# Optimization experiments

Hardware: AMD Instinct MI355X
Metric: run time of the kernel (lower is better)

## Reference

```python
import jax, jax.numpy as jnp
import numpy as np

S, B, C, H, M = 384, 8, 1024, 16, 1536
CC = C // H


def setup_inputs() -> dict:
    key = jax.random.key(0)
    ks = jax.random.split(key, 8)
    x = jax.random.normal(ks[0], (S, B, C), dtype=jnp.float32)
    pe = jax.random.normal(ks[1], (S, B, C), dtype=jnp.float32)
    memory_k = jax.random.normal(ks[2], (M, B, H, CC), dtype=jnp.float32)
    memory_v = jax.random.normal(ks[3], (M, B, H, CC), dtype=jnp.float32)
    w_qkv = jax.random.normal(ks[4], (C, 3 * C), dtype=jnp.float32) * 0.02
    b_qkv = jnp.zeros((3 * C,), dtype=jnp.float32)
    w_out = jax.random.normal(ks[5], (C, C), dtype=jnp.float32) * 0.02
    b_out = jnp.zeros((C,), dtype=jnp.float32)
    terminal = jnp.zeros((B,), dtype=bool)
    # causal mask over the new tokens: True = masked (future positions)
    content_mask = jnp.broadcast_to(
        (jnp.arange(S)[None, :] > jnp.arange(S)[:, None])[:, :, None], (S, S, B))
    padding_mask = jnp.zeros((S, B), dtype=bool)  # True = padded
    memory_length = jax.random.randint(ks[6], (B,), 0, M, dtype=jnp.int32)
    return dict(x=x, positional_encoding=pe, memory_k=memory_k, memory_v=memory_v,
                w_qkv=w_qkv, b_qkv=b_qkv, w_out=w_out, b_out=b_out,
                terminal=terminal, content_mask=content_mask,
                padding_mask=padding_mask, memory_length=memory_length)


def reference(x, positional_encoding, memory_k, memory_v, w_qkv, b_qkv,
              w_out, b_out, terminal, content_mask, padding_mask, memory_length):
    s, b, c = x.shape
    # qkv projection
    qkv = (x + positional_encoding) @ w_qkv + b_qkv          # [s,b,3c]
    q, k, v = jnp.split(qkv, 3, axis=-1)
    q = q.reshape(s, b, H, CC)
    k = k.reshape(s, b, H, CC)
    v = v.reshape(s, b, H, CC)
    # clear_memory(terminal): zero lengths for terminal episodes
    mem_len = jnp.where(terminal, 0, memory_length)          # [b]
    # ragged memory concat expressed with fixed capacity M + padding mask
    k_full = jnp.concatenate([memory_k, k], axis=0)          # [M+s,b,H,CC]
    v_full = jnp.concatenate([memory_v, v], axis=0)
    mem_pad = jnp.arange(M)[:, None] >= mem_len[None, :]     # [M,b] True=masked
    kv_pad = jnp.concatenate([mem_pad, padding_mask], axis=0)  # [M+s,b]
    mem_content = jnp.zeros((s, M, b), dtype=bool)           # memory visible to all queries
    full_content = jnp.concatenate([mem_content, content_mask], axis=1)  # [s,M+s,b]
    mask = full_content | kv_pad[None, :, :]                 # [s,M+s,b]
    # attention
    scores = jnp.einsum('sbhc,tbhc->stbh', q, k_full) * (1.0 / np.sqrt(CC))
    scores = jnp.where(mask[:, :, :, None], jnp.float32(-1e9), scores)
    p = jax.nn.softmax(scores, axis=1)                       # [s,M+s,b,h]
    out = jnp.einsum('stbh,tbhc->sbhc', p, v_full).reshape(s, b, c)
    return out @ w_out + b_out
```

## Files before the change

kernel.cpp:

```cpp
#include <hip/hip_runtime.h>
#include <math.h>

#define S_DIM 384
#define B_DIM 8
#define C_DIM 1024
#define H_DIM 16
#define M_DIM 1536
#define CC_DIM 64
#define ROWS  (S_DIM * B_DIM)
#define N3C   (3 * C_DIM)
#define CHUNK 6
#define MAXS  5

typedef unsigned short u16;
typedef short bf8v  __attribute__((ext_vector_type(8)));
typedef short bf4v  __attribute__((ext_vector_type(4)));
typedef u16   us8   __attribute__((ext_vector_type(8)));
typedef u16   us4   __attribute__((ext_vector_type(4)));
typedef float f4v   __attribute__((ext_vector_type(4)));

__device__ __forceinline__ u16 f2bf(float f) {
    unsigned u = __float_as_uint(f);
    u += 0x7fffu + ((u >> 16) & 1u);
    return (u16)(u >> 16);
}
__device__ __forceinline__ float bf2f(u16 v) {
    return __uint_as_float(((unsigned)v) << 16);
}
#if __has_builtin(__builtin_amdgcn_exp2f)
#define EX2(x) __builtin_amdgcn_exp2f(x)
#else
#define EX2(x) __expf((x) * 0.69314718056f)
#endif
#define QSCALE (0.125f * 1.44269504f)

__device__ __forceinline__ f4v mfma16x16x16bf16(bf4v a, bf4v b, f4v c) {
#if __has_builtin(__builtin_amdgcn_mfma_f32_16x16x16bf16_1k)
    return __builtin_amdgcn_mfma_f32_16x16x16bf16_1k(a, b, c, 0, 0, 0);
#else
    return c;
#endif
}

__device__ __forceinline__ void gload16(const u16* g, u16* l) {
    __builtin_amdgcn_global_load_lds(
        (const __attribute__((address_space(1))) void*)g,
        (__attribute__((address_space(3))) void*)l, 16, 0, 0);
}

__device__ __forceinline__ void tr_direct8(const float* __restrict__ in,
                                           u16* __restrict__ out,
                                           int R, int Cc, int r0, int c0, int tid) {
    const int c4 = c0 + (tid & 15) * 4;
    const int rq = r0 + (tid >> 4) * 8;
    float4 L[8];
    #pragma unroll
    for (int k = 0; k < 8; k++)
        L[k] = *(const float4*)(in + (size_t)(rq + k) * Cc + c4);
    #pragma unroll
    for (int j = 0; j < 4; j++) {
        us8 o;
        #pragma unroll
        for (int k = 0; k < 8; k++)
            o[k] = f2bf(((const float*)&L[k])[j]);
        *(us8*)(out + (size_t)(c4 + j) * R + rq) = o;
    }
}

__global__ __launch_bounds__(256) void prep_all(
    const float* __restrict__ x, const float* __restrict__ pe, u16* __restrict__ Abf,
    const float* __restrict__ wqkv, u16* __restrict__ Wqkvt,
    const float* __restrict__ wout, u16* __restrict__ Woutt,
    const float* __restrict__ mk, u16* __restrict__ mk_bf,
    const float* __restrict__ mv, u16* __restrict__ mv_t,
    const unsigned char* __restrict__ terminal, const int* __restrict__ mem_len)
{
    const int bid = blockIdx.x, tid = threadIdx.x;

    if (bid < 1536) {
        const int bh = bid & 127, tg = bid >> 7;
        const int t0 = tg * 128;
        const int b = bh >> 4;
        const int L = terminal[b] ? 0 : mem_len[b];
        const int Lc = ((L + 63) >> 6) << 6;
        if (t0 >= Lc) return;
        const int cc4 = (tid & 15) * 4;
        const int tq = t0 + (tid >> 4) * 8;
        float4 Lv[8];
        #pragma unroll
        for (int k = 0; k < 8; k++)
            Lv[k] = *(const float4*)(mv + ((size_t)(tq + k) * 128 + bh) * 64 + cc4);
        #pragma unroll
        for (int j = 0; j < 4; j++) {
            us8 o;
            #pragma unroll
            for (int k = 0; k < 8; k++)
                o[k] = f2bf(((const float*)&Lv[k])[j]);
            *(us8*)(mv_t + ((size_t)bh * 64 + cc4 + j) * M_DIM + tq) = o;
        }
    } else if (bid < 4608) {
        const int b6 = bid - 1536;
        const int b = b6 & 7, t0 = (b6 >> 3) * 4;
        const int L = terminal[b] ? 0 : mem_len[b];
        const int Lc = ((L + 63) >> 6) << 6;
        if (t0 >= Lc) return;
        const int r = t0 + (tid >> 6);
        const size_t rb = (size_t)r * 8192 + (size_t)b * 1024;
        const int cw = (tid & 63) * 4;
        float4 v[4];
        #pragma unroll
        for (int j = 0; j < 4; j++)
            v[j] = *(const float4*)(mk + rb + cw + j * 256);
        #pragma unroll
        for (int j = 0; j < 4; j++) {
            us4 o;
            o[0] = f2bf(v[j].x); o[1] = f2bf(v[j].y);
            o[2] = f2bf(v[j].z); o[3] = f2bf(v[j].w);
            *(us4*)(mk_bf + rb + cw + j * 256) = o;
        }
    } else if (bid < 5376) {
        size_t i0 = (size_t)(bid - 4608) * 4096 + tid * 16;
        float4 xv[4], pv[4];
        #pragma unroll
        for (int j = 0; j < 4; j++) {
            xv[j] = *(const float4*)(x + i0 + j * 4);
            pv[j] = *(const float4*)(pe + i0 + j * 4);
        }
        #pragma unroll
        for (int h8 = 0; h8 < 2; h8++) {
            us8 o;
            #pragma unroll
            for (int j = 0; j < 2; j++) {
                float4 a = xv[h8 * 2 + j], p = pv[h8 * 2 + j];
                o[j * 4 + 0] = f2bf(a.x + p.x);
                o[j * 4 + 1] = f2bf(a.y + p.y);
                o[j * 4 + 2] = f2bf(a.z + p.z);
                o[j * 4 + 3] = f2bf(a.w + p.w);
            }
            *(us8*)(Abf + i0 + h8 * 8) = o;
        }
    } else if (bid < 5760) {
        const int b2 = bid - 5376;
        tr_direct8(wqkv, Wqkvt, C_DIM, N3C, (b2 / 48) * 128, (b2 % 48) * 64, tid);
    } else {
        const int b3 = bid - 5760;
        tr_direct8(wout, Woutt, C_DIM, C_DIM, (b3 / 16) * 128, (b3 % 16) * 64, tid);
    }
}

__global__ __launch_bounds__(256) void qkv_gemm(
    const u16* __restrict__ Abf, const u16* __restrict__ Wt,
    const float* __restrict__ bias,
    u16* __restrict__ Qw, u16* __restrict__ Kw, u16* __restrict__ Vwt)
{
    __shared__ u16 smem[128 * 64 + 64 * 64];
    u16* As = smem;
    u16* Bs = smem + 128 * 64;
    u16* Cs = smem;

    const int tid = threadIdx.x;
    const int lane = tid & 63, w = tid >> 6;
    const int lr = lane & 15, quad = lane >> 4;
    const int wm = w >> 1, wn = w & 1;
    const int row0 = blockIdx.y * 128, col0 = blockIdx.x * 64;

    f4v acc[4][2];
    #pragma unroll
    for (int i = 0; i < 4; i++)
        #pragma unroll
        for (int j = 0; j < 2; j++)
            acc[i][j] = (f4v){0.f, 0.f, 0.f, 0.f};

    for (int k0 = 0; k0 < C_DIM; k0 += 64) {
        __syncthreads();
        #pragma unroll
        for (int j = 0; j < 4; j++) {
            int idx = j * 256 + tid;
            int r = idx >> 3, c = (idx & 7) ^ (r & 7);
            gload16(&Abf[(size_t)(row0 + r) * C_DIM + k0 + c * 8], &As[idx * 8]);
        }
        #pragma unroll
        for (int j = 0; j < 2; j++) {
            int idx = j * 256 + tid;
            int r = idx >> 3, c = (idx & 7) ^ (r & 7);
            gload16(&Wt[(size_t)(col0 + r) * C_DIM + k0 + c * 8], &Bs[idx * 8]);
        }
        __syncthreads();
        #pragma unroll
        for (int kh = 0; kh < 2; kh++) {
            bf8v a[4], b[2];
            #pragma unroll
            for (int mi = 0; mi < 4; mi++) {
                int row = wm * 64 + mi * 16 + lr;
                int p = (kh * 4 + quad) ^ (lr & 7);
                a[mi] = *(const bf8v*)&As[row * 64 + p * 8];
            }
            #pragma unroll
            for (int nj = 0; nj < 2; nj++) {
                int row = wn * 32 + nj * 16 + lr;
                int p = (kh * 4 + quad) ^ (lr & 7);
                b[nj] = *(const bf8v*)&Bs[row * 64 + p * 8];
            }
            #pragma unroll
            for (int mi = 0; mi < 4; mi++)
                #pragma unroll
                for (int nj = 0; nj < 2; nj++)
                    acc[mi][nj] = __builtin_amdgcn_mfma_f32_16x16x32_bf16(a[mi], b[nj], acc[mi][nj], 0, 0, 0);
        }
    }

    const int which = col0 >> 10;
    const int h = (col0 >> 6) & 15;
    const float qs = (which == 0) ? QSCALE : 1.0f;

    __syncthreads();
    #pragma unroll
    for (int nj = 0; nj < 2; nj++) {
        int col = col0 + wn * 32 + nj * 16 + lr;
        float bv = bias[col];
        #pragma unroll
        for (int mi = 0; mi < 4; mi++)
            #pragma unroll
            for (int reg = 0; reg < 4; reg++)
                Cs[(wm * 64 + mi * 16 + quad * 4 + reg) * 72 + wn * 32 + nj * 16 + lr] =
                    f2bf((acc[mi][nj][reg] + bv) * qs);
    }
    __syncthreads();

    if (which != 2) {
        u16* dstbuf = (which == 0) ? Qw : Kw;
        int r = tid >> 1, half = tid & 1;
        int rg = row0 + r, s = rg >> 3, bb = rg & 7;
        u16* drow = dstbuf + ((size_t)(bb * 16 + h) * S_DIM + s) * 64 + half * 32;
        #pragma unroll
        for (int i = 0; i < 4; i++)
            *(us8*)(drow + i * 8) = *(const us8*)&Cs[r * 72 + half * 32 + i * 8];
    } else {
        int cc = tid & 63, w4 = tid >> 6;
        int s0 = row0 >> 3;
        #pragma unroll
        for (int pb = 0; pb < 2; pb++) {
            int bb = w4 * 2 + pb;
            us8 v0, v1;
            #pragma unroll
            for (int sl = 0; sl < 8; sl++) {
                v0[sl] = Cs[(sl * 8 + bb) * 72 + cc];
                v1[sl] = Cs[((sl + 8) * 8 + bb) * 72 + cc];
            }
            u16* dr = Vwt + ((size_t)(bb * 16 + h) * 64 + cc) * S_DIM + s0;
            *(us8*)dr = v0;
            *(us8*)(dr + 8) = v1;
        }
    }
}

__global__ __launch_bounds__(256) void attn_split(
    const u16* __restrict__ Qw, const u16* __restrict__ Kw,
    const u16* __restrict__ mk_bf, const u16* __restrict__ Vwt,
    const u16* __restrict__ mv_t, const unsigned char* __restrict__ terminal,
    const int* __restrict__ mem_len, u16* __restrict__ Op, float* __restrict__ ml)
{
    __shared__ u16 KsAll[2][64 * 64];
    __shared__ u16 VsAll[2][64 * 64];

    const int tid = threadIdx.x;
    const int lane = tid & 63, w = tid >> 6;
    const int lr = lane & 15, quad = lane >> 4, q8 = quad * 8;
    const int bid = blockIdx.x;
    const int j = bid % MAXS;
    const int g = bid / MAXS;
    const int b = g & 7, h = (g >> 3) & 15, sc = g >> 7;
    const int bh = b * 16 + h, sq0 = sc * 64;
    const int L = terminal[b] ? 0 : mem_len[b];
    const int memChunks = (L + 63) >> 6;
    const int total = memChunks + sc + 1;
    const int lo = j * CHUNK;
    const int hi = (lo + CHUNK < total) ? lo + CHUNK : total;
    if (lo >= total) return;

    const int qrow = sq0 + w * 16 + lr;

    const u16* qbase = Qw + ((size_t)bh * S_DIM + sq0 + w * 16 + lr) * 64;
    bf8v qf0 = *(const bf8v*)&qbase[q8];
    bf8v qf1 = *(const bf8v*)&qbase[32 + q8];

    f4v O[4];
    #pragma unroll
    for (int nj = 0; nj < 4; nj++) O[nj] = (f4v){0.f, 0.f, 0.f, 0.f};
    float m_i = -1e30f, l_i = 0.0f;

    const f4v zero = (f4v){0.f, 0.f, 0.f, 0.f};

    auto stagef = [&](int ch, int buf) {
        const bool isMem = (ch < memChunks);
        const int tloc = isMem ? ch * 64 : (ch - memChunks) * 64;
        const u16* kb; size_t kstr;
        if (isMem) { kb = mk_bf + ((size_t)tloc * 128 + bh) * 64; kstr = 128 * 64; }
        else       { kb = Kw + ((size_t)bh * S_DIM + tloc) * 64; kstr = 64; }
        const u16* vb; size_t vstr;
        if (isMem) { vb = mv_t + (size_t)bh * 64 * M_DIM + tloc; vstr = M_DIM; }
        else       { vb = Vwt + (size_t)bh * 64 * S_DIM + tloc; vstr = S_DIM; }
        #pragma unroll
        for (int jj = 0; jj < 2; jj++) {
            int idx = jj * 256 + tid;
            int r = idx >> 3, c = (idx & 7) ^ (r & 7);
            gload16(kb + (size_t)r * kstr + c * 8, &KsAll[buf][idx * 8]);
        }
        #pragma unroll
        for (int jj = 0; jj < 2; jj++) {
            int idx = jj * 256 + tid;
            int cc = idx >> 3, c = (idx & 7) ^ (cc & 7);
            gload16(vb + (size_t)cc * vstr + c * 8, &VsAll[buf][idx * 8]);
        }
    };

    int cur = 0;
    stagef(lo, 0);

    for (int ch = lo; ch < hi; ch++) {
        if (ch + 1 < hi) {
            stagef(ch + 1, cur ^ 1);
            asm volatile("s_waitcnt vmcnt(4)" ::: "memory");
        } else {
            asm volatile("s_waitcnt vmcnt(0)" ::: "memory");
        }
        __builtin_amdgcn_sched_barrier(0);
        __builtin_amdgcn_s_barrier();
        __builtin_amdgcn_sched_barrier(0);

        const u16* Ks = &KsAll[cur][0];
        const u16* Vs = &VsAll[cur][0];
        const bool isMem = (ch < memChunks);
        const int tloc = isMem ? ch * 64 : (ch - memChunks) * 64;

        f4v sv[4];
        __builtin_amdgcn_s_setprio(1);
        #pragma unroll
        for (int tt = 0; tt < 4; tt++) {
            int row = tt * 16 + lr;
            int p0 = quad ^ (lr & 7), p1 = (4 + quad) ^ (lr & 7);
            bf8v k0 = *(const bf8v*)&Ks[row * 64 + p0 * 8];
            bf8v k1 = *(const bf8v*)&Ks[row * 64 + p1 * 8];
            sv[tt] = __builtin_amdgcn_mfma_f32_16x16x32_bf16(k0, qf0, zero, 0, 0, 0);
            sv[tt] = __builtin_amdgcn_mfma_f32_16x16x32_bf16(k1, qf1, sv[tt], 0, 0, 0);
        }
        __builtin_amdgcn_s_setprio(0);

        if (isMem) {
            if (tloc + 64 > L) {
                #pragma unroll
                for (int tt = 0; tt < 4; tt++)
                    #pragma unroll
                    for (int reg = 0; reg < 4; reg++) {
                        int t = tloc + tt * 16 + quad * 4 + reg;
                        if (t >= L) sv[tt][reg] = -1e30f;
                    }
            }
        } else {
            if (tloc + 63 > sq0 + w * 16) {
                #pragma unroll
                for (int tt = 0; tt < 4; tt++)
                    #pragma unroll
                    for (int reg = 0; reg < 4; reg++) {
                        int t = tloc + tt * 16 + quad * 4 + reg;
                        if (t > qrow) sv[tt][reg] = -1e30f;
                    }
            }
        }

        float rowmax = fmaxf(fmaxf(sv[0][0], sv[0][1]), fmaxf(sv[0][2], sv[0][3]));
        #pragma unroll
        for (int tt = 1; tt < 4; tt++)
            rowmax = fmaxf(rowmax, fmaxf(fmaxf(sv[tt][0], sv[tt][1]),
                                         fmaxf(sv[tt][2], sv[tt][3])));
        rowmax = fmaxf(rowmax, __shfl_xor(rowmax, 16));
        rowmax = fmaxf(rowmax, __shfl_xor(rowmax, 32));
        float mnew = fmaxf(m_i, rowmax);
        float alpha = EX2(m_i - mnew);
        m_i = mnew;
        float sum = 0.0f;
        bf4v pf[4];
        #pragma unroll
        for (int tt = 0; tt < 4; tt++) {
            #pragma unroll
            for (int reg = 0; reg < 4; reg++) {
                float p = EX2(sv[tt][reg] - mnew);
                sum += p;
                pf[tt][reg] = (short)f2bf(p);
            }
        }
        sum += __shfl_xor(sum, 16);
        sum += __shfl_xor(sum, 32);
        l_i = l_i * alpha + sum;

        float alphaR[4];
        #pragma unroll
        for (int reg = 0; reg < 4; reg++)
            alphaR[reg] = __shfl(alpha, quad * 4 + reg);
        #pragma unroll
        for (int nj = 0; nj < 4; nj++)
            #pragma unroll
            for (int reg = 0; reg < 4; reg++)
                O[nj][reg] *= alphaR[reg];

        __builtin_amdgcn_s_setprio(1);
        #pragma unroll
        for (int tt = 0; tt < 4; tt++) {
            #pragma unroll
            for (int nj = 0; nj < 4; nj++) {
                int cc = nj * 16 + lr;
                int c = (tt * 2 + (quad >> 1)) ^ (lr & 7);
                bf4v vf = *(const bf4v*)&Vs[cc * 64 + c * 8 + (quad & 1) * 4];
                O[nj] = mfma16x16x16bf16(pf[tt], vf, O[nj]);
            }
        }
        __builtin_amdgcn_s_setprio(0);

        __builtin_amdgcn_sched_barrier(0);
        __builtin_amdgcn_s_barrier();
        cur ^= 1;
    }

    const size_t pbase = (size_t)(g * MAXS + j) * 64;
    if (quad == 0) {
        int row = w * 16 + lr;
        float2 mlv = {m_i, l_i};
        *(float2*)&ml[(pbase + row) * 2] = mlv;
    }
    #pragma unroll
    for (int reg = 0; reg < 4; reg++) {
        int row = w * 16 + quad * 4 + reg;
        #pragma unroll
        for (int nj = 0; nj < 4; nj++)
            Op[(pbase + row) * 64 + nj * 16 + lr] = f2bf(O[nj][reg]);
    }
}

__global__ __launch_bounds__(256) void attn_combine(
    const unsigned char* __restrict__ terminal, const int* __restrict__ mem_len,
    const u16* __restrict__ Op, const float* __restrict__ ml, u16* __restrict__ Obf)
{
    const int g = blockIdx.x;
    const int b = g & 7, h = (g >> 3) & 15, sc = g >> 7;
    const int tid = threadIdx.x;
    const int row = tid >> 2, c0 = (tid & 3) * 16;

    const int L = terminal[b] ? 0 : mem_len[b];
    const int total = ((L + 63) >> 6) + sc + 1;
    const int nsp = (total + CHUNK - 1) / CHUNK;

    float m[MAXS], lv[MAXS];
    #pragma unroll
    for (int j = 0; j < MAXS; j++) {
        if (j < nsp) {
            size_t base = (size_t)(g * MAXS + j) * 64 + row;
            m[j]  = ml[base * 2];
            lv[j] = ml[base * 2 + 1];
        } else { m[j] = -1e30f; lv[j] = 0.0f; }
    }
    float mstar = m[0];
    #pragma unroll
    for (int j = 1; j < MAXS; j++) mstar = fmaxf(mstar, m[j]);
    float sc_j[MAXS], l = 0.0f;
    #pragma unroll
    for (int j = 0; j < MAXS; j++) {
        sc_j[j] = (j < nsp) ? EX2(m[j] - mstar) : 0.0f;
        l += sc_j[j] * lv[j];
    }
    float inv = 1.0f / l;

    float o[16];
    #pragma unroll
    for (int c = 0; c < 16; c++) o[c] = 0.0f;
    for (int j = 0; j < nsp; j++) {
        const u16* src = &Op[((size_t)(g * MAXS + j) * 64 + row) * 64 + c0];
        us8 v0 = *(const us8*)src;
        us8 v1 = *(const us8*)(src + 8);
        #pragma unroll
        for (int c = 0; c < 8; c++) {
            o[c]     += sc_j[j] * bf2f(v0[c]);
            o[c + 8] += sc_j[j] * bf2f(v1[c]);
        }
    }
    int s = sc * 64 + row;
    size_t dst = ((size_t)s * 8 + b) * C_DIM + h * 64 + c0;
    us8 w0, w1;
    #pragma unroll
    for (int c = 0; c < 8; c++) {
        w0[c] = f2bf(o[c] * inv);
        w1[c] = f2bf(o[c + 8] * inv);
    }
    *(us8*)&Obf[dst] = w0;
    *(us8*)&Obf[dst + 8] = w1;
}

__global__ __launch_bounds__(256) void proj_gemm(
    const u16* __restrict__ Abf, const u16* __restrict__ Wt,
    const float* __restrict__ bias, float* __restrict__ out)
{
    __shared__ u16 As[64 * 64];
    __shared__ u16 Bs[64 * 64];
    const int tid = threadIdx.x;
    const int lane = tid & 63, w = tid >> 6;
    const int lr = lane & 15, quad = lane >> 4;
    const int row0 = blockIdx.y * 64, col0 = blockIdx.x * 64;

    f4v acc[4];
    #pragma unroll
    for (int i = 0; i < 4; i++) acc[i] = (f4v){0.f, 0.f, 0.f, 0.f};

    for (int k0 = 0; k0 < C_DIM; k0 += 64) {
        __syncthreads();
        #pragma unroll
        for (int j = 0; j < 2; j++) {
            int idx = j * 256 + tid;
            int r = idx >> 3, c = (idx & 7) ^ (r & 7);
            gload16(&Abf[(size_t)(row0 + r) * C_DIM + k0 + c * 8], &As[idx * 8]);
            gload16(&Wt[(size_t)(col0 + r) * C_DIM + k0 + c * 8], &Bs[idx * 8]);
        }
        __syncthreads();
        #pragma unroll
        for (int kh = 0; kh < 2; kh++) {
            int p = (kh * 4 + quad) ^ (lr & 7);
            bf8v a = *(const bf8v*)&As[(w * 16 + lr) * 64 + p * 8];
            #pragma unroll
            for (int nj = 0; nj < 4; nj++) {
                bf8v bfr = *(const bf8v*)&Bs[(nj * 16 + lr) * 64 + p * 8];
                acc[nj] = __builtin_amdgcn_mfma_f32_16x16x32_bf16(a, bfr, acc[nj], 0, 0, 0);
            }
        }
    }

    #pragma unroll
    for (int nj = 0; nj < 4; nj++) {
        int col = col0 + nj * 16 + lr;
        float bv = bias[col];
        #pragma unroll
        for (int reg = 0; reg < 4; reg++) {
            int rg = row0 + w * 16 + quad * 4 + reg;
            out[(size_t)rg * C_DIM + col] = acc[nj][reg] + bv;
        }
    }
}

extern "C" void kernel_launch(void* const* d_in, const int* in_sizes, int n_in,
                              void* d_out, int out_size, void* d_ws, size_t ws_size,
                              hipStream_t stream) {
    const float* x    = (const float*)d_in[0];
    const float* pe   = (const float*)d_in[1];
    const float* mk   = (const float*)d_in[2];
    const float* mv   = (const float*)d_in[3];
    const float* wqkv = (const float*)d_in[4];
    const float* bqkv = (const float*)d_in[5];
    const float* wout = (const float*)d_in[6];
    const float* bout = (const float*)d_in[7];
    const unsigned char* term = (const unsigned char*)d_in[8];
    const int* mem_len = (const int*)d_in[11];

    char* ws = (char*)d_ws;
    u16* Abf   = (u16*)(ws + 0);
    u16* Obf   = (u16*)(ws + 0);
    u16* Wqkvt = (u16*)(ws + 6291456);
    float* ml  = (float*)(ws + 6291456);
    u16* Woutt = (u16*)(ws + 12582912);
    u16* mk_bf = (u16*)(ws + 14680064);
    u16* mv_t  = (u16*)(ws + 39845888);
    u16* Qw    = (u16*)(ws + 65011712);
    u16* Kw    = (u16*)(ws + 71303168);
    u16* Vwt   = (u16*)(ws + 77594624);
    u16* Op    = (u16*)(ws + 83886080);

    float* out = (float*)d_out;

    prep_all<<<5888, 256, 0, stream>>>(x, pe, Abf, wqkv, Wqkvt, wout, Woutt,
                                       mk, mk_bf, mv, mv_t, term, mem_len);

    qkv_gemm<<<dim3(N3C / 64, ROWS / 128), 256, 0, stream>>>(
        Abf, Wqkvt, bqkv, Qw, Kw, Vwt);

    attn_split<<<B_DIM * H_DIM * (S_DIM / 64) * MAXS, 256, 0, stream>>>(
        Qw, Kw, mk_bf, Vwt, mv_t, term, mem_len, Op, ml);

    attn_combine<<<B_DIM * H_DIM * (S_DIM / 64), 256, 0, stream>>>(
        term, mem_len, Op, ml, Obf);

    proj_gemm<<<dim3(C_DIM / 64, ROWS / 64), 256, 0, stream>>>(
        Obf, Woutt, bout, out);
}
```

Baseline: 282.6 us.

## Deepen attention K/V prefetch ring and defer online-softmax rescaling

Widens the split attention kernel's LDS staging from double to quad buffering. Chunks are now prefetched two iterations ahead, and the end-of-iteration barrier is dropped because the ring size keeps buffers from being overwritten while still in use. It also adds lazy softmax rescaling: the running max and the O/l rescale are updated only when some row's max grows by more than 8 (log2 domain), so most chunks skip the alpha shuffle and multiply. Smaller changes use the packed v_cvt_pk_bf16_f32 instruction for probability conversion and 32-bit address arithmetic in staging, at the cost of twice the LDS footprint and bounded unnormalised growth in the accumulators.

Result: slower. 289.6 us (+2.5%).

```diff
diff --git a/kernel.cpp b/kernel.cpp
--- a/kernel.cpp
+++ b/kernel.cpp
@@ -34,6 +34,12 @@
 #endif
 #define QSCALE (0.125f * 1.44269504f)
 
+__device__ __forceinline__ unsigned cvtpk_bf16(float a, float b) {
+    unsigned r;
+    asm("v_cvt_pk_bf16_f32 %0, %1, %2" : "=v"(r) : "v"(a), "v"(b));
+    return r;
+}
+
 __device__ __forceinline__ f4v mfma16x16x16bf16(bf4v a, bf4v b, f4v c) {
 #if __has_builtin(__builtin_amdgcn_mfma_f32_16x16x16bf16_1k)
     return __builtin_amdgcn_mfma_f32_16x16x16bf16_1k(a, b, c, 0, 0, 0);
@@ -260,8 +266,8 @@
     const u16* __restrict__ mv_t, const unsigned char* __restrict__ terminal,
     const int* __restrict__ mem_len, u16* __restrict__ Op, float* __restrict__ ml)
 {
-    __shared__ u16 KsAll[2][64 * 64];
-    __shared__ u16 VsAll[2][64 * 64];
+    __shared__ u16 KsAll[4][64 * 64];
+    __shared__ u16 VsAll[4][64 * 64];
 
     const int tid = threadIdx.x;
     const int lane = tid & 63, w = tid >> 6;
@@ -294,32 +300,36 @@
     auto stagef = [&](int ch, int buf) {
         const bool isMem = (ch < memChunks);
         const int tloc = isMem ? ch * 64 : (ch - memChunks) * 64;
-        const u16* kb; size_t kstr;
-        if (isMem) { kb = mk_bf + ((size_t)tloc * 128 + bh) * 64; kstr = 128 * 64; }
-        else       { kb = Kw + ((size_t)bh * S_DIM + tloc) * 64; kstr = 64; }
-        const u16* vb; size_t vstr;
+        const u16* kb; unsigned kstr;
+        if (isMem) { kb = mk_bf + ((size_t)tloc * 128 + bh) * 64; kstr = 128u * 64u; }
+        else       { kb = Kw + ((size_t)bh * S_DIM + tloc) * 64; kstr = 64u; }
+        const u16* vb; unsigned vstr;
         if (isMem) { vb = mv_t + (size_t)bh * 64 * M_DIM + tloc; vstr = M_DIM; }
         else       { vb = Vwt + (size_t)bh * 64 * S_DIM + tloc; vstr = S_DIM; }
+        u16* KsB = &KsAll[buf][0];
+        u16* VsB = &VsAll[buf][0];
         #pragma unroll
         for (int jj = 0; jj < 2; jj++) {
             int idx = jj * 256 + tid;
-            int r = idx >> 3, c = (idx & 7) ^ (r & 7);
-            gload16(kb + (size_t)r * kstr + c * 8, &KsAll[buf][idx * 8]);
+            unsigned r = idx >> 3, c = (idx & 7) ^ (r & 7);
+            gload16(kb + r * kstr + c * 8u, &KsB[idx * 8]);
         }
         #pragma unroll
         for (int jj = 0; jj < 2; jj++) {
             int idx = jj * 256 + tid;
-            int cc = idx >> 3, c = (idx & 7) ^ (cc & 7);
-            gload16(vb + (size_t)cc * vstr + c * 8, &VsAll[buf][idx * 8]);
+            unsigned cc = idx >> 3, c = (idx & 7) ^ (cc & 7);
+            gload16(vb + cc * vstr + c * 8u, &VsB[idx * 8]);
         }
     };
 
-    int cur = 0;
     stagef(lo, 0);
+    if (lo + 1 < hi) stagef(lo + 1, 1);
 
     for (int ch = lo; ch < hi; ch++) {
-        if (ch + 1 < hi) {
-            stagef(ch + 1, cur ^ 1);
+        if (ch + 2 < hi) {
+            stagef(ch + 2, (ch + 2 - lo) & 3);
+            asm volatile("s_waitcnt vmcnt(8)" ::: "memory");
+        } else if (ch + 1 < hi) {
             asm volatile("s_waitcnt vmcnt(4)" ::: "memory");
         } else {
             asm volatile("s_waitcnt vmcnt(0)" ::: "memory");
@@ -328,8 +338,8 @@
         __builtin_amdgcn_s_barrier();
         __builtin_amdgcn_sched_barrier(0);
 
-        const u16* Ks = &KsAll[cur][0];
-        const u16* Vs = &VsAll[cur][0];
+        const u16* Ks = &KsAll[(ch - lo) & 3][0];
+        const u16* Vs = &VsAll[(ch - lo) & 3][0];
         const bool isMem = (ch < memChunks);
         const int tloc = isMem ? ch * 64 : (ch - memChunks) * 64;
 
@@ -375,33 +385,50 @@
                                          fmaxf(sv[tt][2], sv[tt][3])));
         rowmax = fmaxf(rowmax, __shfl_xor(rowmax, 16));
         rowmax = fmaxf(rowmax, __shfl_xor(rowmax, 32));
-        float mnew = fmaxf(m_i, rowmax);
-        float alpha = EX2(m_i - mnew);
-        m_i = mnew;
-        float sum = 0.0f;
-        bf4v pf[4];
+
+        const bool defer = __all(rowmax - m_i <= 8.0f);
+        const float mnew = defer ? m_i : fmaxf(m_i, rowmax);
+
+        float p[16];
+        float s0 = 0.f, s1 = 0.f, s2 = 0.f, s3 = 0.f;
         #pragma unroll
         for (int tt = 0; tt < 4; tt++) {
-            #pragma unroll
-            for (int reg = 0; reg < 4; reg++) {
-                float p = EX2(sv[tt][reg] - mnew);
-                sum += p;
-                pf[tt][reg] = (short)f2bf(p);
-            }
-        }
+            p[tt * 4 + 0] = EX2(sv[tt][0] - mnew);
+            p[tt * 4 + 1] = EX2(sv[tt][1] - mnew);
+            p[tt * 4 + 2] = EX2(sv[tt][2] - mnew);
+            p[tt * 4 + 3] = EX2(sv[tt][3] - mnew);
+            s0 += p[tt * 4 + 0]; s1 += p[tt * 4 + 1];
+            s2 += p[tt * 4 + 2]; s3 += p[tt * 4 + 3];
+        }
+        float sum = (s0 + s1) + (s2 + s3);
         sum += __shfl_xor(sum, 16);
         sum += __shfl_xor(sum, 32);
-        l_i = l_i * alpha + sum;
-
-        float alphaR[4];
-        #pragma unroll
-        for (int reg = 0; reg < 4; reg++)
-            alphaR[reg] = __shfl(alpha, quad * 4 + reg);
-        #pragma unroll
-        for (int nj = 0; nj < 4; nj++)
+
+        bf4v pf[4];
+        #pragma unroll
+        for (int tt = 0; tt < 4; tt++) {
+            union { bf4v v; unsigned u[2]; } pu;
+            pu.u[0] = cvtpk_bf16(p[tt * 4 + 0], p[tt * 4 + 1]);
+            pu.u[1] = cvtpk_bf16(p[tt * 4 + 2], p[tt * 4 + 3]);
+            pf[tt] = pu.v;
+        }
+
+        if (defer) {
+            l_i += sum;
+        } else {
+            float alpha = EX2(m_i - mnew);
+            m_i = mnew;
+            l_i = l_i * alpha + sum;
+            float alphaR[4];
             #pragma unroll
             for (int reg = 0; reg < 4; reg++)
-                O[nj][reg] *= alphaR[reg];
+                alphaR[reg] = __shfl(alpha, quad * 4 + reg);
+            #pragma unroll
+            for (int nj = 0; nj < 4; nj++)
+                #pragma unroll
+                for (int reg = 0; reg < 4; reg++)
+                    O[nj][reg] *= alphaR[reg];
+        }
 
         __builtin_amdgcn_s_setprio(1);
         #pragma unroll
@@ -415,10 +442,6 @@
             }
         }
         __builtin_amdgcn_s_setprio(0);
-
-        __builtin_amdgcn_sched_barrier(0);
-        __builtin_amdgcn_s_barrier();
-        cur ^= 1;
     }
 
     const size_t pbase = (size_t)(g * MAXS + j) * 64;
```
